# Optimization experiments

Hardware: AMD Instinct MI355X
Metric: run time of the kernel (lower is better)

## Reference

```python
import jax, jax.numpy as jnp
import numpy as np

N, IN, HID, H, OUT, G = 2048, 128, 128, 4, 10, 8
NEG_SLOPE = 0.2
THRESHOLD = 0.0


def setup_inputs() -> dict:
    key = jax.random.key(0)
    ks = jax.random.split(key, 18)
    s = 0.05
    return {
        "x": jax.random.normal(ks[0], (N, IN), jnp.float32),
        "attn_tensor": jax.random.normal(ks[1], (12, N, N), jnp.float32),
        "batch_idx": jnp.sort(jax.random.randint(ks[2], (N,), 0, G)),
        "conv_w": jax.random.normal(ks[3], (12,), jnp.float32) * s,
        "conv_b": jnp.zeros((), jnp.float32),
        "W1": jax.random.normal(ks[4], (IN, H * HID), jnp.float32) * s,
        "att_src1": jax.random.normal(ks[5], (H, HID), jnp.float32) * s,
        "att_dst1": jax.random.normal(ks[6], (H, HID), jnp.float32) * s,
        "att_edge1": jax.random.normal(ks[7], (H, HID), jnp.float32) * s,
        "We1": jax.random.normal(ks[8], (H * HID,), jnp.float32) * s,
        "b1": jnp.zeros((H * HID,), jnp.float32),
        "W2": jax.random.normal(ks[9], (H * HID, HID), jnp.float32) * s,
        "att_src2": jax.random.normal(ks[10], (1, HID), jnp.float32) * s,
        "att_dst2": jax.random.normal(ks[11], (1, HID), jnp.float32) * s,
        "att_edge2": jax.random.normal(ks[12], (1, HID), jnp.float32) * s,
        "We2": jax.random.normal(ks[13], (HID,), jnp.float32) * s,
        "b2": jnp.zeros((HID,), jnp.float32),
        "fc_w": jax.random.normal(ks[14], (HID, OUT), jnp.float32) * s,
        "fc_b": jnp.zeros((OUT,), jnp.float32),
    }


def gat_layer(x, adj, eattr, W, a_src, a_dst, a_edge, We, b, heads, out_ch):
    n = x.shape[0]
    h = (x @ W).reshape(n, heads, out_ch)            # [N,H,C]
    s_src = jnp.einsum('nhc,hc->nh', h, a_src)       # alpha contribution of source node
    s_dst = jnp.einsum('nhc,hc->nh', h, a_dst)       # alpha contribution of target node
    c_e = jnp.einsum('hc,hc->h', a_edge, We.reshape(heads, out_ch))  # scalar edge coeff per head
    # logits[s,t,h] for message s -> t (edge (s,t) means agg_mat[s,t] > thr)
    logits = s_src[:, None, :] + s_dst[None, :, :] + eattr[:, :, None] * c_e[None, None, :]
    logits = jnp.where(logits >= 0, logits, NEG_SLOPE * logits)  # leaky_relu(0.2)
    logits = jnp.where(adj[:, :, None], logits, -1e9)
    alpha = jax.nn.softmax(logits, axis=0)           # segment softmax over sources per target
    out = jnp.einsum('sth,shc->thc', alpha, h).reshape(n, heads * out_ch)
    return out + b


def reference(x, attn_tensor, batch_idx, conv_w, conv_b,
              W1, att_src1, att_dst1, att_edge1, We1, b1,
              W2, att_src2, att_dst2, att_edge2, We2, b2,
              fc_w, fc_b):
    # 1x1 conv over 12 attention channels -> dense [N,N] aggregated matrix
    agg = jnp.einsum('c,cst->st', conv_w, attn_tensor) + conv_b
    eye = jnp.eye(N, dtype=bool)
    mask_off = (agg > THRESHOLD) & (~eye)            # PyG GATConv removes then re-adds self loops
    # self-loop edge_attr = mean of incoming edge attrs per target (fill_value='mean')
    cnt = mask_off.sum(axis=0)
    mean_attr = jnp.where(mask_off, agg, 0.0).sum(axis=0) / jnp.maximum(cnt, 1)
    eattr = jnp.where(mask_off, agg, 0.0) + jnp.diag(mean_attr)
    adj = mask_off | eye

    h = gat_layer(x, adj, eattr, W1, att_src1, att_dst1, att_edge1, We1, b1, H, HID)
    h = jax.nn.relu(h)
    h = gat_layer(h, adj, eattr, W2, att_src2, att_dst2, att_edge2, We2, b2, 1, HID)

    sums = jax.ops.segment_sum(h, batch_idx, num_segments=G)
    counts = jax.ops.segment_sum(jnp.ones((N,), h.dtype), batch_idx, num_segments=G)
    pooled = sums / jnp.maximum(counts, 1.0)[:, None]  # global_mean_pool
    return jax.nn.log_softmax(pooled @ fc_w + fc_b, axis=1)
```

## Files before the change

### kernel.cpp

```cpp
#include <hip/hip_runtime.h>
#include <hip/hip_bf16.h>
#include <math.h>

#define NN 2048
#define NEG_SLOPE 0.2f

typedef __attribute__((ext_vector_type(8))) short bf16x8;
typedef __attribute__((ext_vector_type(4))) float f32x4;

static __device__ inline short f2bf(float x) {
  union { float f; unsigned u; } v;
  v.f = x;
  unsigned r = v.u + 0x7fffu + ((v.u >> 16) & 1u);
  return (short)(r >> 16);
}

__global__ __launch_bounds__(256) void k_pre(
    const float* __restrict__ attn, const float* __restrict__ conv_w,
    const float* __restrict__ conv_b, const float* __restrict__ W1,
    const float* __restrict__ W2, const float* __restrict__ ae1,
    const float* __restrict__ We1, const float* __restrict__ ae2,
    const float* __restrict__ We2, float* __restrict__ aggT,
    __hip_bfloat16* __restrict__ w1t, __hip_bfloat16* __restrict__ w2t,
    float* __restrict__ zreg, float* __restrict__ ce) {
  const int b = blockIdx.x;
  const int tid = threadIdx.x;
  if (b < 1024) {
    __shared__ float tile[64][68];
    const int t0 = (b & 31) * 64;
    const int s0 = (b >> 5) * 64;
    const int sl = tid >> 4;
    const int t4 = (tid & 15) * 4;
    float w[12];
#pragma unroll
    for (int c = 0; c < 12; ++c) w[c] = conv_w[c];
    const float cb = conv_b[0];
    f32x4 acc[4];
#pragma unroll
    for (int k = 0; k < 4; ++k) acc[k] = (f32x4){cb, cb, cb, cb};
    for (int c = 0; c < 12; ++c) {
      const float* base =
          attn + (size_t)c * NN * NN + (size_t)(s0 + sl) * NN + t0 + t4;
#pragma unroll
      for (int k = 0; k < 4; ++k)
        acc[k] += w[c] * *(const f32x4*)(base + (size_t)k * 16 * NN);
    }
#pragma unroll
    for (int k = 0; k < 4; ++k) *(f32x4*)&tile[sl + 16 * k][t4] = acc[k];
    __syncthreads();
    const int tl = tid >> 2;
    const int sq = (tid & 3) * 16;
    float* orow = aggT + (size_t)(t0 + tl) * NN + s0 + sq;
#pragma unroll
    for (int g = 0; g < 4; ++g) {
      f32x4 v = {tile[sq + 4 * g][tl], tile[sq + 4 * g + 1][tl],
                 tile[sq + 4 * g + 2][tl], tile[sq + 4 * g + 3][tl]};
      *(f32x4*)(orow + 4 * g) = v;
    }
  } else if (b < 1056) {
#pragma unroll
    for (int k = 0; k < 8; ++k) {
      int o = (b - 1024) * 2048 + k * 256 + tid;
      ((short*)w1t)[o] = f2bf(W1[(o & 127) * 512 + (o >> 7)]);
    }
  } else if (b < 1088) {
#pragma unroll
    for (int k = 0; k < 8; ++k) {
      int o = (b - 1056) * 2048 + k * 256 + tid;
      ((short*)w2t)[o] = f2bf(W2[(o & 511) * 128 + (o >> 9)]);
    }
  } else if (b < 1108) {
    int i = (b - 1088) * 1024 + tid * 4;
    *(f32x4*)(zreg + i) = (f32x4){0.f, 0.f, 0.f, 0.f};
  } else {
    const int lane = tid & 63;
    const int wv = tid >> 6;
    float q1 = ae1[wv * 128 + lane] * We1[wv * 128 + lane] +
               ae1[wv * 128 + 64 + lane] * We1[wv * 128 + 64 + lane];
    for (int off = 32; off; off >>= 1) q1 += __shfl_down(q1, off);
    if (lane == 0) ce[wv] = q1;
    float q2 = ae2[lane] * We2[lane] + ae2[64 + lane] * We2[64 + lane];
    for (int off = 32; off; off >>= 1) q2 += __shfl_down(q2, off);
    if (tid == 0) ce[4] = q2;
  }
}

__global__ __launch_bounds__(256) void k_gemm1(
    const float* __restrict__ x, const __hip_bfloat16* __restrict__ w1t,
    const float* __restrict__ asrc1, const float* __restrict__ adst1,
    __hip_bfloat16* __restrict__ hTsw1, float* __restrict__ ssrc1,
    float* __restrict__ sdst1) {
  const int tid = threadIdx.x;
  const int w = (int)blockIdx.x * 4 + (tid >> 6);
  const int lane = tid & 63, row = lane & 15, kg = lane >> 4;
  const int mb = w >> 4, nb = w & 15;
  const int m0 = mb * 16, n0 = nb * 32;
  const float* axrow = x + (size_t)(m0 + row) * 128 + kg * 8;
  f32x4 acc[2];
#pragma unroll
  for (int f = 0; f < 2; ++f) acc[f] = (f32x4){0.f, 0.f, 0.f, 0.f};
#pragma unroll
  for (int ks = 0; ks < 4; ++ks) {
    f32x4 xa = *(const f32x4*)(axrow + ks * 32);
    f32x4 xb = *(const f32x4*)(axrow + ks * 32 + 4);
    bf16x8 Af = {f2bf(xa[0]), f2bf(xa[1]), f2bf(xa[2]), f2bf(xa[3]),
                 f2bf(xb[0]), f2bf(xb[1]), f2bf(xb[2]), f2bf(xb[3])};
#pragma unroll
    for (int f = 0; f < 2; ++f) {
      bf16x8 Bf = *(const bf16x8*)(w1t + (size_t)(n0 + f * 16 + row) * 128 +
                                   kg * 8 + ks * 32);
      acc[f] = __builtin_amdgcn_mfma_f32_16x16x32_bf16(Af, Bf, acc[f], 0, 0, 0);
    }
  }
  const int h = nb >> 2;
  float as[2], ad[2];
#pragma unroll
  for (int f = 0; f < 2; ++f) {
    int ch = (n0 + f * 16 + row) & 127;
    as[f] = asrc1[h * 128 + ch];
    ad[f] = adst1[h * 128 + ch];
  }
  float ps[4] = {0.f, 0.f, 0.f, 0.f}, pd[4] = {0.f, 0.f, 0.f, 0.f};
#pragma unroll
  for (int f = 0; f < 2; ++f)
#pragma unroll
    for (int r = 0; r < 4; ++r) {
      ps[r] += acc[f][r] * as[f];
      pd[r] += acc[f][r] * ad[f];
    }
#pragma unroll
  for (int m = 1; m < 16; m <<= 1) {
#pragma unroll
    for (int r = 0; r < 4; ++r) {
      ps[r] += __shfl_xor(ps[r], m);
      pd[r] += __shfl_xor(pd[r], m);
    }
  }
  if (row == 0) {
#pragma unroll
    for (int r = 0; r < 4; ++r) {
      int node = m0 + kg * 4 + r;
      atomicAdd(&ssrc1[node * 4 + h], ps[r]);
      atomicAdd(&sdst1[node * 4 + h], pd[r]);
    }
  }
#pragma unroll
  for (int f = 0; f < 2; ++f) {
    const int cbi = nb * 2 + f;
    short4 ct;
    ct.x = f2bf(acc[f][0]); ct.y = f2bf(acc[f][1]);
    ct.z = f2bf(acc[f][2]); ct.w = f2bf(acc[f][3]);
    size_t a4 = (size_t)cbi * (NN * 16) +
                (size_t)(((m0 >> 3) + (kg >> 1)) * 128 + row * 8 + (kg & 1) * 4);
    *(short4*)((short*)hTsw1 + a4) = ct;
  }
}

__global__ __launch_bounds__(256) void k_attn1(
    const float* __restrict__ aggT, const __hip_bfloat16* __restrict__ hTsw1,
    const float* __restrict__ ssrc1, const float* __restrict__ sdst1,
    const float* __restrict__ ce_all, const float* __restrict__ b1,
    __hip_bfloat16* __restrict__ feat1b) {
  const int tid = threadIdx.x;
  const int t0 = (int)(blockIdx.x >> 2) * 16;
  const int h = (int)(blockIdx.x & 3u);
  __shared__ float ss_sh[2048];
  __shared__ float red[4][16][128];
  __shared__ float den_sh[4][16];
  __shared__ float st_sum[4][16];
  __shared__ float st_cnt[4][16];
  for (int i = tid; i < 2048; i += 256) ss_sh[i] = ssrc1[i * 4 + h];
  __syncthreads();
  const int lane = tid & 63, w = tid >> 6, row = lane & 15, kg = lane >> 4;
  const int sbeg = w * 512;
  const int tRow = t0 + row;
  const float* arow = aggT + (size_t)tRow * NN;
  {
    float psum = 0.f, pcnt = 0.f;
    for (int s0 = sbeg; s0 < sbeg + 512; s0 += 32) {
      const int sk = s0 + kg * 8;
      f32x4 a0 = *(const f32x4*)(arow + sk);
      f32x4 a1 = *(const f32x4*)(arow + sk + 4);
      float av[8] = {a0[0], a0[1], a0[2], a0[3], a1[0], a1[1], a1[2], a1[3]};
#pragma unroll
      for (int j = 0; j < 8; ++j) {
        bool m = (av[j] > 0.f) && (sk + j != tRow);
        psum += m ? av[j] : 0.f;
        pcnt += m ? 1.f : 0.f;
      }
    }
    psum += __shfl_xor(psum, 16); psum += __shfl_xor(psum, 32);
    pcnt += __shfl_xor(pcnt, 16); pcnt += __shfl_xor(pcnt, 32);
    if (lane < 16) { st_sum[w][lane] = psum; st_cnt[w][lane] = pcnt; }
  }
  __syncthreads();
  const float ma_t =
      (st_sum[0][row] + st_sum[1][row] + st_sum[2][row] + st_sum[3][row]) /
      fmaxf(st_cnt[0][row] + st_cnt[1][row] + st_cnt[2][row] + st_cnt[3][row],
            1.f);
  const float ce = ce_all[h];
  const float sd_t = sdst1[tRow * 4 + h];
  const float* ssh = ss_sh + sbeg;
  const __hip_bfloat16* bbase =
      hTsw1 + (size_t)(h * 8) * (NN * 16) + kg * 128 + row * 8;
  f32x4 acc[8];
#pragma unroll
  for (int f = 0; f < 8; ++f) acc[f] = (f32x4){0.f, 0.f, 0.f, 0.f};
  float dpart = 0.f;
  for (int s0 = sbeg; s0 < sbeg + 512; s0 += 32) {
    const int sk = s0 + kg * 8;
    f32x4 a0 = *(const f32x4*)(arow + sk);
    f32x4 a1 = *(const f32x4*)(arow + sk + 4);
    f32x4 sv0 = *(const f32x4*)(ssh + (sk - sbeg));
    f32x4 sv1 = *(const f32x4*)(ssh + (sk - sbeg) + 4);
    float av[8] = {a0[0], a0[1], a0[2], a0[3], a1[0], a1[1], a1[2], a1[3]};
    float sv[8] = {sv0[0], sv0[1], sv0[2], sv0[3],
                   sv1[0], sv1[1], sv1[2], sv1[3]};
    short pb[8];
#pragma unroll
    for (int j = 0; j < 8; ++j) {
      const int s = sk + j;
      const float a = av[j];
      const bool diag = (s == tRow);
      const float ev = diag ? ma_t : a;
      const bool adj = diag || (a > 0.f);
      float l = sv[j] + sd_t + ev * ce;
      l = fmaxf(l, NEG_SLOPE * l);
      const float pv = adj ? __expf(l) : 0.f;
      dpart += pv;
      pb[j] = f2bf(pv);
    }
    bf16x8 A = {pb[0], pb[1], pb[2], pb[3], pb[4], pb[5], pb[6], pb[7]};
    const __hip_bfloat16* bp = bbase + (size_t)s0 * 16;
#pragma unroll
    for (int f = 0; f < 8; ++f) {
      bf16x8 B = *(const bf16x8*)(bp + (size_t)f * (NN * 16));
      acc[f] = __builtin_amdgcn_mfma_f32_16x16x32_bf16(A, B, acc[f], 0, 0, 0);
    }
  }
  dpart += __shfl_xor(dpart, 16);
  dpart += __shfl_xor(dpart, 32);
  __syncthreads();
#pragma unroll
  for (int f = 0; f < 8; ++f)
#pragma unroll
    for (int r = 0; r < 4; ++r) red[w][kg * 4 + r][f * 16 + row] = acc[f][r];
  if (lane < 16) den_sh[w][lane] = dpart;
  __syncthreads();
#pragma unroll
  for (int i = 0; i < 8; ++i) {
    int idx = i * 256 + tid;
    int t = idx >> 7, c = idx & 127;
    float nsum = red[0][t][c] + red[1][t][c] + red[2][t][c] + red[3][t][c];
    float dsum = den_sh[0][t] + den_sh[1][t] + den_sh[2][t] + den_sh[3][t];
    float v = nsum / dsum + b1[h * 128 + c];
    feat1b[(size_t)(t0 + t) * 512 + h * 128 + c] =
        __float2bfloat16(v > 0.f ? v : 0.f);
  }
}

__global__ __launch_bounds__(256) void k_gemm2(
    const __hip_bfloat16* __restrict__ feat1b,
    const __hip_bfloat16* __restrict__ w2t, const float* __restrict__ asrc2,
    const float* __restrict__ adst2, __hip_bfloat16* __restrict__ hTsw2,
    float* __restrict__ ssrc2, float* __restrict__ sdst2) {
  const int tid = threadIdx.x;
  const int w = (int)blockIdx.x * 4 + (tid >> 6);
  const int lane = tid & 63, row = lane & 15, kg = lane >> 4;
  const int mb = w >> 2, nb = w & 3;
  const int m0 = mb * 16, n0 = nb * 32;
  const __hip_bfloat16* arow = feat1b + (size_t)(m0 + row) * 512 + kg * 8;
  f32x4 acc[2];
#pragma unroll
  for (int f = 0; f < 2; ++f) acc[f] = (f32x4){0.f, 0.f, 0.f, 0.f};
#pragma unroll
  for (int ks = 0; ks < 16; ++ks) {
    bf16x8 Af = *(const bf16x8*)(arow + ks * 32);
#pragma unroll
    for (int f = 0; f < 2; ++f) {
      bf16x8 Bf = *(const bf16x8*)(w2t + (size_t)(n0 + f * 16 + row) * 512 +
                                   kg * 8 + ks * 32);
      acc[f] = __builtin_amdgcn_mfma_f32_16x16x32_bf16(Af, Bf, acc[f], 0, 0, 0);
    }
  }
  float as[2], ad[2];
#pragma unroll
  for (int f = 0; f < 2; ++f) {
    int ch = (n0 + f * 16 + row) & 127;
    as[f] = asrc2[ch];
    ad[f] = adst2[ch];
  }
  float ps[4] = {0.f, 0.f, 0.f, 0.f}, pd[4] = {0.f, 0.f, 0.f, 0.f};
#pragma unroll
  for (int f = 0; f < 2; ++f)
#pragma unroll
    for (int r = 0; r < 4; ++r) {
      ps[r] += acc[f][r] * as[f];
      pd[r] += acc[f][r] * ad[f];
    }
#pragma unroll
  for (int m = 1; m < 16; m <<= 1) {
#pragma unroll
    for (int r = 0; r < 4; ++r) {
      ps[r] += __shfl_xor(ps[r], m);
      pd[r] += __shfl_xor(pd[r], m);
    }
  }
  if (row == 0) {
#pragma unroll
    for (int r = 0; r < 4; ++r) {
      int node = m0 + kg * 4 + r;
      atomicAdd(&ssrc2[node], ps[r]);
      atomicAdd(&sdst2[node], pd[r]);
    }
  }
#pragma unroll
  for (int f = 0; f < 2; ++f) {
    const int cbi = nb * 2 + f;
    short4 ct;
    ct.x = f2bf(acc[f][0]); ct.y = f2bf(acc[f][1]);
    ct.z = f2bf(acc[f][2]); ct.w = f2bf(acc[f][3]);
    size_t a4 = (size_t)cbi * (NN * 16) +
                (size_t)(((m0 >> 3) + (kg >> 1)) * 128 + row * 8 + (kg & 1) * 4);
    *(short4*)((short*)hTsw2 + a4) = ct;
  }
}

__global__ __launch_bounds__(256) void k_attn2(
    const float* __restrict__ aggT, const __hip_bfloat16* __restrict__ hTsw2,
    const float* __restrict__ ssrc2, const float* __restrict__ sdst2,
    const float* __restrict__ ce_all, const float* __restrict__ b2,
    float* __restrict__ feat2) {
  const int tid = threadIdx.x;
  const int t0 = (int)blockIdx.x * 16;
  __shared__ float ss_sh[2048];
  __shared__ float red[4][16][128];
  __shared__ float den_sh[4][16];
  __shared__ float st_sum[4][16];
  __shared__ float st_cnt[4][16];
  for (int i = tid; i < 2048; i += 256) ss_sh[i] = ssrc2[i];
  __syncthreads();
  const int lane = tid & 63, w = tid >> 6, row = lane & 15, kg = lane >> 4;
  const int sbeg = w * 512;
  const int tRow = t0 + row;
  const float* arow = aggT + (size_t)tRow * NN;
  {
    float psum = 0.f, pcnt = 0.f;
    for (int s0 = sbeg; s0 < sbeg + 512; s0 += 32) {
      const int sk = s0 + kg * 8;
      f32x4 a0 = *(const f32x4*)(arow + sk);
      f32x4 a1 = *(const f32x4*)(arow + sk + 4);
      float av[8] = {a0[0], a0[1], a0[2], a0[3], a1[0], a1[1], a1[2], a1[3]};
#pragma unroll
      for (int j = 0; j < 8; ++j) {
        bool m = (av[j] > 0.f) && (sk + j != tRow);
        psum += m ? av[j] : 0.f;
        pcnt += m ? 1.f : 0.f;
      }
    }
    psum += __shfl_xor(psum, 16); psum += __shfl_xor(psum, 32);
    pcnt += __shfl_xor(pcnt, 16); pcnt += __shfl_xor(pcnt, 32);
    if (lane < 16) { st_sum[w][lane] = psum; st_cnt[w][lane] = pcnt; }
  }
  __syncthreads();
  const float ma_t =
      (st_sum[0][row] + st_sum[1][row] + st_sum[2][row] + st_sum[3][row]) /
      fmaxf(st_cnt[0][row] + st_cnt[1][row] + st_cnt[2][row] + st_cnt[3][row],
            1.f);
  const float ce = ce_all[4];
  const float sd_t = sdst2[tRow];
  const float* ssh = ss_sh + sbeg;
  const __hip_bfloat16* bbase = hTsw2 + kg * 128 + row * 8;
  f32x4 acc[8];
#pragma unroll
  for (int f = 0; f < 8; ++f) acc[f] = (f32x4){0.f, 0.f, 0.f, 0.f};
  float dpart = 0.f;
  for (int s0 = sbeg; s0 < sbeg + 512; s0 += 32) {
    const int sk = s0 + kg * 8;
    f32x4 a0 = *(const f32x4*)(arow + sk);
    f32x4 a1 = *(const f32x4*)(arow + sk + 4);
    f32x4 sv0 = *(const f32x4*)(ssh + (sk - sbeg));
    f32x4 sv1 = *(const f32x4*)(ssh + (sk - sbeg) + 4);
    float av[8] = {a0[0], a0[1], a0[2], a0[3], a1[0], a1[1], a1[2], a1[3]};
    float sv[8] = {sv0[0], sv0[1], sv0[2], sv0[3],
                   sv1[0], sv1[1], sv1[2], sv1[3]};
    short pb[8];
#pragma unroll
    for (int j = 0; j < 8; ++j) {
      const int s = sk + j;
      const float a = av[j];
      const bool diag = (s == tRow);
      const float ev = diag ? ma_t : a;
      const bool adj = diag || (a > 0.f);
      float l = sv[j] + sd_t + ev * ce;
      l = fmaxf(l, NEG_SLOPE * l);
      const float pv = adj ? __expf(l) : 0.f;
      dpart += pv;
      pb[j] = f2bf(pv);
    }
    bf16x8 A = {pb[0], pb[1], pb[2], pb[3], pb[4], pb[5], pb[6], pb[7]};
    const __hip_bfloat16* bp = bbase + (size_t)s0 * 16;
#pragma unroll
    for (int f = 0; f < 8; ++f) {
      bf16x8 B = *(const bf16x8*)(bp + (size_t)f * (NN * 16));
      acc[f] = __builtin_amdgcn_mfma_f32_16x16x32_bf16(A, B, acc[f], 0, 0, 0);
    }
  }
  dpart += __shfl_xor(dpart, 16);
  dpart += __shfl_xor(dpart, 32);
  __syncthreads();
#pragma unroll
  for (int f = 0; f < 8; ++f)
#pragma unroll
    for (int r = 0; r < 4; ++r) red[w][kg * 4 + r][f * 16 + row] = acc[f][r];
  if (lane < 16) den_sh[w][lane] = dpart;
  __syncthreads();
#pragma unroll
  for (int i = 0; i < 8; ++i) {
    int idx = i * 256 + tid;
    int t = idx >> 7, c = idx & 127;
    float nsum = red[0][t][c] + red[1][t][c] + red[2][t][c] + red[3][t][c];
    float dsum = den_sh[0][t] + den_sh[1][t] + den_sh[2][t] + den_sh[3][t];
    feat2[(size_t)(t0 + t) * 128 + c] = nsum / dsum + b2[c];
  }
}

__global__ __launch_bounds__(256) void k_poolhead(
    const float* __restrict__ feat, const int* __restrict__ bidx,
    const float* __restrict__ fcw, const float* __restrict__ fcb,
    float* __restrict__ out) {
  const int g = blockIdx.x;
  const int tid = threadIdx.x;
  __shared__ int lo[2];
  __shared__ float ps2[256];
  __shared__ float lsh[10];
  if (tid == 0) { lo[0] = NN; lo[1] = NN; }
  __syncthreads();
  for (int n = tid; n < NN; n += 256) {
    int b = bidx[n];
    int bprev = (n == 0) ? -1 : bidx[n - 1];
    if (b >= g && bprev < g) atomicMin(&lo[0], n);
    if (b >= g + 1 && bprev < g + 1) atomicMin(&lo[1], n);
  }
  __syncthreads();
  int s = lo[0], e = lo[1];
  const int c = tid & 127, half = tid >> 7;
  float sum = 0.f;
  for (int n = s + half; n < e; n += 2) sum += feat[(size_t)n * 128 + c];
  ps2[tid] = sum;
  __syncthreads();
  if (tid < 128) {
    float cntf = (float)((e - s) > 1 ? (e - s) : 1);
    ps2[tid] = (ps2[tid] + ps2[tid + 128]) / cntf;
  }
  __syncthreads();
  if (tid < 10) {
    float v = fcb[tid];
    for (int ch = 0; ch < 128; ++ch) v += ps2[ch] * fcw[ch * 10 + tid];
    lsh[tid] = v;
  }
  __syncthreads();
  if (tid < 10) {
    float m = -1e30f;
    for (int i = 0; i < 10; ++i) m = fmaxf(m, lsh[i]);
    float den = 0.f;
    for (int i = 0; i < 10; ++i) den += expf(lsh[i] - m);
    out[g * 10 + tid] = lsh[tid] - m - logf(den);
  }
}

extern "C" void kernel_launch(void* const* d_in, const int* in_sizes, int n_in,
                              void* d_out, int out_size, void* d_ws,
                              size_t ws_size, hipStream_t stream) {
  (void)in_sizes; (void)n_in; (void)out_size; (void)ws_size;
  const float* x      = (const float*)d_in[0];
  const float* attn   = (const float*)d_in[1];
  const int*   bidx   = (const int*)d_in[2];
  const float* conv_w = (const float*)d_in[3];
  const float* conv_b = (const float*)d_in[4];
  const float* W1     = (const float*)d_in[5];
  const float* asrc1  = (const float*)d_in[6];
  const float* adst1  = (const float*)d_in[7];
  const float* aedge1 = (const float*)d_in[8];
  const float* We1    = (const float*)d_in[9];
  const float* b1     = (const float*)d_in[10];
  const float* W2     = (const float*)d_in[11];
  const float* asrc2  = (const float*)d_in[12];
  const float* adst2  = (const float*)d_in[13];
  const float* aedge2 = (const float*)d_in[14];
  const float* We2    = (const float*)d_in[15];
  const float* b2     = (const float*)d_in[16];
  const float* fcw    = (const float*)d_in[17];
  const float* fcb    = (const float*)d_in[18];

  float* ws = (float*)d_ws;
  float* aggT  = ws;
  float* feat2 = aggT + 4194304;
  float* ssrc1 = feat2 + 262144;
  float* sdst1 = ssrc1 + 8192;
  float* ssrc2 = sdst1 + 8192;
  float* sdst2 = ssrc2 + 2048;
  float* ce    = sdst2 + 2048;
  float* bf    = ce + 64;
  __hip_bfloat16* w1t    = (__hip_bfloat16*)bf;
  __hip_bfloat16* w2t    = (__hip_bfloat16*)(bf + 32768);
  __hip_bfloat16* hTsw1  = (__hip_bfloat16*)(bf + 65536);
  __hip_bfloat16* hTsw2  = (__hip_bfloat16*)(bf + 589824);
  __hip_bfloat16* feat1b = (__hip_bfloat16*)(bf + 720896);

  k_pre<<<1109, 256, 0, stream>>>(attn, conv_w, conv_b, W1, W2, aedge1, We1,
                                  aedge2, We2, aggT, w1t, w2t, ssrc1, ce);
  k_gemm1<<<512, 256, 0, stream>>>(x, w1t, asrc1, adst1, hTsw1, ssrc1, sdst1);
  k_attn1<<<512, 256, 0, stream>>>(aggT, hTsw1, ssrc1, sdst1, ce, b1, feat1b);
  k_gemm2<<<128, 256, 0, stream>>>(feat1b, w2t, asrc2, adst2, hTsw2, ssrc2,
                                   sdst2);
  k_attn2<<<128, 256, 0, stream>>>(aggT, hTsw2, ssrc2, sdst2, ce, b2, feat2);
  k_poolhead<<<8, 256, 0, stream>>>(feat2, bidx, fcw, fcb, (float*)d_out);
}
```

Baseline: 147.6 us.

## Fuse self-loop mean stats into conv pass, drop atomics, split attn2 channels

Computes the per-target masked sum and count used for the self-loop edge attribute inside the conv/transpose pre-pass, writing per-tile partials that both attention kernels reduce. This removes the extra full read of each aggT row that k_attn1 and k_attn2 each did before. It also replaces the atomicAdd accumulation of attention scores with deterministic partial buffers, so the zero-fill blocks are no longer needed. k_attn2 is split across two channel halves to double its block count and improve occupancy, at the cost of recomputing the exp logits twice.

```diff
diff --git a/kernel.cpp b/kernel.cpp
--- a/kernel.cpp
+++ b/kernel.cpp
@@ -21,8 +21,9 @@
     const float* __restrict__ W2, const float* __restrict__ ae1,
     const float* __restrict__ We1, const float* __restrict__ ae2,
     const float* __restrict__ We2, float* __restrict__ aggT,
+    float* __restrict__ ssum_part, float* __restrict__ scnt_part,
     __hip_bfloat16* __restrict__ w1t, __hip_bfloat16* __restrict__ w2t,
-    float* __restrict__ zreg, float* __restrict__ ce) {
+    float* __restrict__ ce) {
   const int b = blockIdx.x;
   const int tid = threadIdx.x;
   if (b < 1024) {
@@ -50,12 +51,27 @@
     __syncthreads();
     const int tl = tid >> 2;
     const int sq = (tid & 3) * 16;
-    float* orow = aggT + (size_t)(t0 + tl) * NN + s0 + sq;
+    const int tglob = t0 + tl;
+    float* orow = aggT + (size_t)tglob * NN + s0 + sq;
+    float psum = 0.f, pcnt = 0.f;
 #pragma unroll
     for (int g = 0; g < 4; ++g) {
       f32x4 v = {tile[sq + 4 * g][tl], tile[sq + 4 * g + 1][tl],
                  tile[sq + 4 * g + 2][tl], tile[sq + 4 * g + 3][tl]};
       *(f32x4*)(orow + 4 * g) = v;
+#pragma unroll
+      for (int j = 0; j < 4; ++j) {
+        int sglob = s0 + sq + 4 * g + j;
+        bool m = (v[j] > 0.f) && (sglob != tglob);
+        psum += m ? v[j] : 0.f;
+        pcnt += m ? 1.f : 0.f;
+      }
+    }
+    psum += __shfl_down(psum, 1); psum += __shfl_down(psum, 2);
+    pcnt += __shfl_down(pcnt, 1); pcnt += __shfl_down(pcnt, 2);
+    if ((tid & 3) == 0) {
+      ssum_part[(b >> 5) * NN + tglob] = psum;
+      scnt_part[(b >> 5) * NN + tglob] = pcnt;
     }
   } else if (b < 1056) {
 #pragma unroll
@@ -69,9 +85,6 @@
       int o = (b - 1056) * 2048 + k * 256 + tid;
       ((short*)w2t)[o] = f2bf(W2[(o & 511) * 128 + (o >> 9)]);
     }
-  } else if (b < 1108) {
-    int i = (b - 1088) * 1024 + tid * 4;
-    *(f32x4*)(zreg + i) = (f32x4){0.f, 0.f, 0.f, 0.f};
   } else {
     const int lane = tid & 63;
     const int wv = tid >> 6;
@@ -88,8 +101,8 @@
 __global__ __launch_bounds__(256) void k_gemm1(
     const float* __restrict__ x, const __hip_bfloat16* __restrict__ w1t,
     const float* __restrict__ asrc1, const float* __restrict__ adst1,
-    __hip_bfloat16* __restrict__ hTsw1, float* __restrict__ ssrc1,
-    float* __restrict__ sdst1) {
+    __hip_bfloat16* __restrict__ hTsw1, float* __restrict__ sspart1,
+    float* __restrict__ sdpart1) {
   const int tid = threadIdx.x;
   const int w = (int)blockIdx.x * 4 + (tid >> 6);
   const int lane = tid & 63, row = lane & 15, kg = lane >> 4;
@@ -140,8 +153,8 @@
 #pragma unroll
     for (int r = 0; r < 4; ++r) {
       int node = m0 + kg * 4 + r;
-      atomicAdd(&ssrc1[node * 4 + h], ps[r]);
-      atomicAdd(&sdst1[node * 4 + h], pd[r]);
+      sspart1[nb * NN + node] = ps[r];
+      sdpart1[nb * NN + node] = pd[r];
     }
   }
 #pragma unroll
@@ -158,7 +171,8 @@
 
 __global__ __launch_bounds__(256) void k_attn1(
     const float* __restrict__ aggT, const __hip_bfloat16* __restrict__ hTsw1,
-    const float* __restrict__ ssrc1, const float* __restrict__ sdst1,
+    const float* __restrict__ sspart1, const float* __restrict__ sdpart1,
+    const float* __restrict__ ssum_part, const float* __restrict__ scnt_part,
     const float* __restrict__ ce_all, const float* __restrict__ b1,
     __hip_bfloat16* __restrict__ feat1b) {
   const int tid = threadIdx.x;
@@ -167,39 +181,26 @@
   __shared__ float ss_sh[2048];
   __shared__ float red[4][16][128];
   __shared__ float den_sh[4][16];
-  __shared__ float st_sum[4][16];
-  __shared__ float st_cnt[4][16];
-  for (int i = tid; i < 2048; i += 256) ss_sh[i] = ssrc1[i * 4 + h];
+  for (int i = tid; i < 2048; i += 256)
+    ss_sh[i] = sspart1[(4 * h + 0) * NN + i] + sspart1[(4 * h + 1) * NN + i] +
+               sspart1[(4 * h + 2) * NN + i] + sspart1[(4 * h + 3) * NN + i];
   __syncthreads();
   const int lane = tid & 63, w = tid >> 6, row = lane & 15, kg = lane >> 4;
   const int sbeg = w * 512;
   const int tRow = t0 + row;
   const float* arow = aggT + (size_t)tRow * NN;
-  {
-    float psum = 0.f, pcnt = 0.f;
-    for (int s0 = sbeg; s0 < sbeg + 512; s0 += 32) {
-      const int sk = s0 + kg * 8;
-      f32x4 a0 = *(const f32x4*)(arow + sk);
-      f32x4 a1 = *(const f32x4*)(arow + sk + 4);
-      float av[8] = {a0[0], a0[1], a0[2], a0[3], a1[0], a1[1], a1[2], a1[3]};
-#pragma unroll
-      for (int j = 0; j < 8; ++j) {
-        bool m = (av[j] > 0.f) && (sk + j != tRow);
-        psum += m ? av[j] : 0.f;
-        pcnt += m ? 1.f : 0.f;
-      }
-    }
-    psum += __shfl_xor(psum, 16); psum += __shfl_xor(psum, 32);
-    pcnt += __shfl_xor(pcnt, 16); pcnt += __shfl_xor(pcnt, 32);
-    if (lane < 16) { st_sum[w][lane] = psum; st_cnt[w][lane] = pcnt; }
-  }
-  __syncthreads();
-  const float ma_t =
-      (st_sum[0][row] + st_sum[1][row] + st_sum[2][row] + st_sum[3][row]) /
-      fmaxf(st_cnt[0][row] + st_cnt[1][row] + st_cnt[2][row] + st_cnt[3][row],
-            1.f);
+  float msum = 0.f, mcnt = 0.f;
+#pragma unroll
+  for (int q = 0; q < 32; ++q) {
+    msum += ssum_part[q * NN + tRow];
+    mcnt += scnt_part[q * NN + tRow];
+  }
+  const float ma_t = msum / fmaxf(mcnt, 1.f);
   const float ce = ce_all[h];
-  const float sd_t = sdst1[tRow * 4 + h];
+  const float sd_t = sdpart1[(4 * h + 0) * NN + tRow] +
+                     sdpart1[(4 * h + 1) * NN + tRow] +
+                     sdpart1[(4 * h + 2) * NN + tRow] +
+                     sdpart1[(4 * h + 3) * NN + tRow];
   const float* ssh = ss_sh + sbeg;
   const __hip_bfloat16* bbase =
       hTsw1 + (size_t)(h * 8) * (NN * 16) + kg * 128 + row * 8;
@@ -265,10 +266,12 @@
     const float* __restrict__ adst2, __hip_bfloat16* __restrict__ hTsw2,
     float* __restrict__ ssrc2, float* __restrict__ sdst2) {
   const int tid = threadIdx.x;
-  const int w = (int)blockIdx.x * 4 + (tid >> 6);
+  const int wv = tid >> 6;
+  const int w = (int)blockIdx.x * 4 + wv;
   const int lane = tid & 63, row = lane & 15, kg = lane >> 4;
   const int mb = w >> 2, nb = w & 3;
   const int m0 = mb * 16, n0 = nb * 32;
+  __shared__ float sred[2][4][16];
   const __hip_bfloat16* arow = feat1b + (size_t)(m0 + row) * 512 + kg * 8;
   f32x4 acc[2];
 #pragma unroll
@@ -309,10 +312,18 @@
   if (row == 0) {
 #pragma unroll
     for (int r = 0; r < 4; ++r) {
-      int node = m0 + kg * 4 + r;
-      atomicAdd(&ssrc2[node], ps[r]);
-      atomicAdd(&sdst2[node], pd[r]);
-    }
+      sred[0][wv][kg * 4 + r] = ps[r];
+      sred[1][wv][kg * 4 + r] = pd[r];
+    }
+  }
+  __syncthreads();
+  if (tid < 16) {
+    float s = sred[0][0][tid] + sred[0][1][tid] + sred[0][2][tid] +
+              sred[0][3][tid];
+    float d = sred[1][0][tid] + sred[1][1][tid] + sred[1][2][tid] +
+              sred[1][3][tid];
+    ssrc2[(int)blockIdx.x * 16 + tid] = s;
+    sdst2[(int)blockIdx.x * 16 + tid] = d;
   }
 #pragma unroll
   for (int f = 0; f < 2; ++f) {
@@ -329,51 +340,36 @@
 __global__ __launch_bounds__(256) void k_attn2(
     const float* __restrict__ aggT, const __hip_bfloat16* __restrict__ hTsw2,
     const float* __restrict__ ssrc2, const float* __restrict__ sdst2,
+    const float* __restrict__ ssum_part, const float* __restrict__ scnt_part,
     const float* __restrict__ ce_all, const float* __restrict__ b2,
     float* __restrict__ feat2) {
   const int tid = threadIdx.x;
-  const int t0 = (int)blockIdx.x * 16;
+  const int t0 = (int)(blockIdx.x >> 1) * 16;
+  const int chalf = (int)(blockIdx.x & 1u);
   __shared__ float ss_sh[2048];
-  __shared__ float red[4][16][128];
+  __shared__ float red[4][16][64];
   __shared__ float den_sh[4][16];
-  __shared__ float st_sum[4][16];
-  __shared__ float st_cnt[4][16];
   for (int i = tid; i < 2048; i += 256) ss_sh[i] = ssrc2[i];
   __syncthreads();
   const int lane = tid & 63, w = tid >> 6, row = lane & 15, kg = lane >> 4;
   const int sbeg = w * 512;
   const int tRow = t0 + row;
   const float* arow = aggT + (size_t)tRow * NN;
-  {
-    float psum = 0.f, pcnt = 0.f;
-    for (int s0 = sbeg; s0 < sbeg + 512; s0 += 32) {
-      const int sk = s0 + kg * 8;
-      f32x4 a0 = *(const f32x4*)(arow + sk);
-      f32x4 a1 = *(const f32x4*)(arow + sk + 4);
-      float av[8] = {a0[0], a0[1], a0[2], a0[3], a1[0], a1[1], a1[2], a1[3]};
-#pragma unroll
-      for (int j = 0; j < 8; ++j) {
-        bool m = (av[j] > 0.f) && (sk + j != tRow);
-        psum += m ? av[j] : 0.f;
-        pcnt += m ? 1.f : 0.f;
-      }
-    }
-    psum += __shfl_xor(psum, 16); psum += __shfl_xor(psum, 32);
-    pcnt += __shfl_xor(pcnt, 16); pcnt += __shfl_xor(pcnt, 32);
-    if (lane < 16) { st_sum[w][lane] = psum; st_cnt[w][lane] = pcnt; }
-  }
-  __syncthreads();
-  const float ma_t =
-      (st_sum[0][row] + st_sum[1][row] + st_sum[2][row] + st_sum[3][row]) /
-      fmaxf(st_cnt[0][row] + st_cnt[1][row] + st_cnt[2][row] + st_cnt[3][row],
-            1.f);
+  float msum = 0.f, mcnt = 0.f;
+#pragma unroll
+  for (int q = 0; q < 32; ++q) {
+    msum += ssum_part[q * NN + tRow];
+    mcnt += scnt_part[q * NN + tRow];
+  }
+  const float ma_t = msum / fmaxf(mcnt, 1.f);
   const float ce = ce_all[4];
   const float sd_t = sdst2[tRow];
   const float* ssh = ss_sh + sbeg;
-  const __hip_bfloat16* bbase = hTsw2 + kg * 128 + row * 8;
-  f32x4 acc[8];
-#pragma unroll
-  for (int f = 0; f < 8; ++f) acc[f] = (f32x4){0.f, 0.f, 0.f, 0.f};
+  const __hip_bfloat16* bbase =
+      hTsw2 + (size_t)(chalf * 4) * (NN * 16) + kg * 128 + row * 8;
+  f32x4 acc[4];
+#pragma unroll
+  for (int f = 0; f < 4; ++f) acc[f] = (f32x4){0.f, 0.f, 0.f, 0.f};
   float dpart = 0.f;
   for (int s0 = sbeg; s0 < sbeg + 512; s0 += 32) {
     const int sk = s0 + kg * 8;
@@ -401,7 +397,7 @@
     bf16x8 A = {pb[0], pb[1], pb[2], pb[3], pb[4], pb[5], pb[6], pb[7]};
     const __hip_bfloat16* bp = bbase + (size_t)s0 * 16;
 #pragma unroll
-    for (int f = 0; f < 8; ++f) {
+    for (int f = 0; f < 4; ++f) {
       bf16x8 B = *(const bf16x8*)(bp + (size_t)f * (NN * 16));
       acc[f] = __builtin_amdgcn_mfma_f32_16x16x32_bf16(A, B, acc[f], 0, 0, 0);
     }
@@ -410,18 +406,19 @@
   dpart += __shfl_xor(dpart, 32);
   __syncthreads();
 #pragma unroll
-  for (int f = 0; f < 8; ++f)
+  for (int f = 0; f < 4; ++f)
 #pragma unroll
     for (int r = 0; r < 4; ++r) red[w][kg * 4 + r][f * 16 + row] = acc[f][r];
   if (lane < 16) den_sh[w][lane] = dpart;
   __syncthreads();
 #pragma unroll
-  for (int i = 0; i < 8; ++i) {
+  for (int i = 0; i < 4; ++i) {
     int idx = i * 256 + tid;
-    int t = idx >> 7, c = idx & 127;
+    int t = idx >> 6, c = idx & 63;
     float nsum = red[0][t][c] + red[1][t][c] + red[2][t][c] + red[3][t][c];
     float dsum = den_sh[0][t] + den_sh[1][t] + den_sh[2][t] + den_sh[3][t];
-    feat2[(size_t)(t0 + t) * 128 + c] = nsum / dsum + b2[c];
+    feat2[(size_t)(t0 + t) * 128 + chalf * 64 + c] =
+        nsum / dsum + b2[chalf * 64 + c];
   }
 }
 
@@ -494,26 +491,32 @@
   const float* fcb    = (const float*)d_in[18];
 
   float* ws = (float*)d_ws;
-  float* aggT  = ws;
-  float* feat2 = aggT + 4194304;
-  float* ssrc1 = feat2 + 262144;
-  float* sdst1 = ssrc1 + 8192;
-  float* ssrc2 = sdst1 + 8192;
-  float* sdst2 = ssrc2 + 2048;
-  float* ce    = sdst2 + 2048;
-  float* bf    = ce + 64;
+  float* aggT      = ws;
+  float* feat2     = aggT + 4194304;
+  float* ssum_part = feat2 + 262144;
+  float* scnt_part = ssum_part + 65536;
+  float* sspart1   = scnt_part + 65536;
+  float* sdpart1   = sspart1 + 32768;
+  float* ssrc2     = sdpart1 + 32768;
+  float* sdst2     = ssrc2 + 2048;
+  float* ce        = sdst2 + 2048;
+  float* bf        = ce + 64;
   __hip_bfloat16* w1t    = (__hip_bfloat16*)bf;
   __hip_bfloat16* w2t    = (__hip_bfloat16*)(bf + 32768);
   __hip_bfloat16* hTsw1  = (__hip_bfloat16*)(bf + 65536);
   __hip_bfloat16* hTsw2  = (__hip_bfloat16*)(bf + 589824);
   __hip_bfloat16* feat1b = (__hip_bfloat16*)(bf + 720896);
 
-  k_pre<<<1109, 256, 0, stream>>>(attn, conv_w, conv_b, W1, W2, aedge1, We1,
-                                  aedge2, We2, aggT, w1t, w2t, ssrc1, ce);
-  k_gemm1<<<512, 256, 0, stream>>>(x, w1t, asrc1, adst1, hTsw1, ssrc1, sdst1);
-  k_attn1<<<512, 256, 0, stream>>>(aggT, hTsw1, ssrc1, sdst1, ce, b1, feat1b);
+  k_pre<<<1089, 256, 0, stream>>>(attn, conv_w, conv_b, W1, W2, aedge1, We1,
+                                  aedge2, We2, aggT, ssum_part, scnt_part, w1t,
+                                  w2t, ce);
+  k_gemm1<<<512, 256, 0, stream>>>(x, w1t, asrc1, adst1, hTsw1, sspart1,
+                                   sdpart1);
+  k_attn1<<<512, 256, 0, stream>>>(aggT, hTsw1, sspart1, sdpart1, ssum_part,
+                                   scnt_part, ce, b1, feat1b);
   k_gemm2<<<128, 256, 0, stream>>>(feat1b, w2t, asrc2, adst2, hTsw2, ssrc2,
                                    sdst2);
-  k_attn2<<<128, 256, 0, stream>>>(aggT, hTsw2, ssrc2, sdst2, ce, b2, feat2);
+  k_attn2<<<256, 256, 0, stream>>>(aggT, hTsw2, ssrc2, sdst2, ssum_part,
+                                   scnt_part, ce, b2, feat2);
   k_poolhead<<<8, 256, 0, stream>>>(feat2, bidx, fcw, fcb, (float*)d_out);
 }
```

Result: faster. 133.3 us (-9.7%).
